# Optimization experiments

Hardware: AMD Instinct MI355X
Metric: run time of the kernel (lower is better)

The kernel has to match this reference:

```python
import jax, jax.numpy as jnp
import numpy as np

UNITS = 768
OUT_STEPS = 64
INPUT_DIM = 96


def setup_inputs() -> dict:
    key = jax.random.key(0)
    ks = jax.random.split(key, 7)
    B, T = 2048, 24
    s_ih = 1.0 / np.sqrt(UNITS)
    inputs = jax.random.normal(ks[0], (B, T, INPUT_DIM), dtype=jnp.float32)
    # PyTorch LSTMCell params: weight_ih [4U, I], weight_hh [4U, U], biases [4U]
    W_ih = jax.random.uniform(ks[1], (4 * UNITS, INPUT_DIM), minval=-s_ih, maxval=s_ih, dtype=jnp.float32)
    W_hh = jax.random.uniform(ks[2], (4 * UNITS, UNITS), minval=-s_ih, maxval=s_ih, dtype=jnp.float32)
    b_ih = jax.random.uniform(ks[3], (4 * UNITS,), minval=-s_ih, maxval=s_ih, dtype=jnp.float32)
    b_hh = jax.random.uniform(ks[4], (4 * UNITS,), minval=-s_ih, maxval=s_ih, dtype=jnp.float32)
    # Dense: Linear(units, input_dim)
    s_d = 1.0 / np.sqrt(UNITS)
    W_d = jax.random.uniform(ks[5], (INPUT_DIM, UNITS), minval=-s_d, maxval=s_d, dtype=jnp.float32)
    b_d = jax.random.uniform(ks[6], (INPUT_DIM,), minval=-s_d, maxval=s_d, dtype=jnp.float32)
    return {"inputs": inputs, "W_ih": W_ih, "W_hh": W_hh, "b_ih": b_ih, "b_hh": b_hh, "W_d": W_d, "b_d": b_d}


def _lstm_cell(x, h, c, W_ih, W_hh, b_ih, b_hh):
    # gates: [B, 4U], PyTorch gate order i, f, g, o
    gates = x @ W_ih.T + b_ih + h @ W_hh.T + b_hh
    i, f, g, o = jnp.split(gates, 4, axis=-1)
    i = jax.nn.sigmoid(i)
    f = jax.nn.sigmoid(f)
    g = jnp.tanh(g)
    o = jax.nn.sigmoid(o)
    c_new = f * c + i * g
    h_new = o * jnp.tanh(c_new)
    return h_new, c_new


def reference(inputs, W_ih, W_hh, b_ih, b_hh, W_d, b_d):
    B = inputs.shape[0]
    h0 = jnp.zeros((B, UNITS), dtype=inputs.dtype)
    c0 = jnp.zeros((B, UNITS), dtype=inputs.dtype)
    # warmup: feed last timestep
    x0 = inputs[:, -1, :]
    h, c = _lstm_cell(x0, h0, c0, W_ih, W_hh, b_ih, b_hh)
    pred0 = h @ W_d.T + b_d

    def step(carry, _):
        pred, h, c = carry
        h2, c2 = _lstm_cell(pred, h, c, W_ih, W_hh, b_ih, b_hh)
        pred2 = h2 @ W_d.T + b_d
        return (pred2, h2, c2), pred2

    _, preds_rest = jax.lax.scan(step, (pred0, h, c), None, length=OUT_STEPS - 1)
    # preds_rest: [out_steps-1, B, I] -> stack with pred0 along time axis 1
    preds = jnp.concatenate([pred0[None], preds_rest], axis=0)  # [out_steps, B, I]
    return jnp.transpose(preds, (1, 0, 2))  # [B, out_steps, I]
```

## Files before the change

### kernel.cpp

```cpp
#include <hip/hip_runtime.h>
#include <hip/hip_bf16.h>
#include <stdint.h>

typedef __hip_bfloat16 bf16_t;
typedef __attribute__((ext_vector_type(4))) float f32x4;
typedef __attribute__((ext_vector_type(8))) short s16x8;

#define UNITS 768
#define NCOLS 3072
#define NPRED 96
#define MROWS 2048

__device__ __forceinline__ float sigf(float x) {
    return __builtin_amdgcn_rcpf(1.f + __expf(-x));
}
__device__ __forceinline__ float tanh_fast(float x) {
    return 1.f - 2.f * __builtin_amdgcn_rcpf(1.f + __expf(2.f * x));
}


__global__ void prep_b0(const float* __restrict__ W_ih, bf16_t* __restrict__ B0T) {
    int idx = blockIdx.x * 256 + threadIdx.x;
    if (idx >= NCOLS * 96) return;
    int c = idx / 96, k = idx % 96;
    int u = ((c >> 6) << 4) + (c & 15);
    int g = (c >> 4) & 3;
    B0T[idx] = (bf16_t)W_ih[(g * UNITS + u) * 96 + k];
}

__global__ void prep_x0(const float* __restrict__ inputs, bf16_t* __restrict__ x0) {
    int idx = blockIdx.x * 256 + threadIdx.x;
    int j = idx & 7;
    int l = (idx >> 3) & 63;
    int fg = idx >> 9;
    int kf = fg % 3;
    int mf = fg / 3;
    int m = mf * 16 + (l & 15);
    int k = kf * 32 + (l >> 4) * 8 + j;
    x0[idx] = (bf16_t)inputs[(m * 24 + 23) * 96 + k];
}

__global__ void prep_bias(const float* __restrict__ b_ih, const float* __restrict__ b_hh,
                          const float* __restrict__ W_ih, const float* __restrict__ b_d,
                          float* __restrict__ b0_r, float* __restrict__ beff_r) {
    int c = blockIdx.x * 256 + threadIdx.x;
    if (c >= NCOLS) return;
    int u = ((c >> 6) << 4) + (c & 15);
    int g = (c >> 4) & 3;
    int r = g * UNITS + u;
    float v = b_ih[r] + b_hh[r];
    float acc = 0.f;
    for (int j = 0; j < 96; ++j) acc += W_ih[r * 96 + j] * b_d[j];
    b0_r[c] = v;
    beff_r[c] = v + acc;
}

__global__ void prep_beff2(const float* __restrict__ W_hh, const float* __restrict__ W_ih,
                           const float* __restrict__ W_d, bf16_t* __restrict__ BeffT) {
    __shared__ float sWih[64][96];
    __shared__ float sWd[96][64];
    const int c0 = blockIdx.x * 64, k0 = blockIdx.y * 64;
    const int tid = threadIdx.x;
    for (int i = tid; i < 64 * 96; i += 256) {
        int cc = i / 96, j = i % 96;
        int c = c0 + cc;
        int u = ((c >> 6) << 4) + (c & 15);
        int g = (c >> 4) & 3;
        sWih[cc][j] = W_ih[(g * UNITS + u) * 96 + j];
    }
    for (int i = tid; i < 96 * 64; i += 256) {
        int j = i / 64, kk = i % 64;
        sWd[j][kk] = W_d[j * UNITS + k0 + kk];
    }
    __syncthreads();
    const int kk = tid & 63;
    const int cc0 = (tid >> 6) * 16;
    for (int cc = cc0; cc < cc0 + 16; ++cc) {
        float acc = 0.f;
#pragma unroll 12
        for (int j = 0; j < 96; ++j) acc += sWih[cc][j] * sWd[j][kk];
        int c = c0 + cc;
        int u = ((c >> 6) << 4) + (c & 15);
        int g = (c >> 4) & 3;
        int r = g * UNITS + u;
        BeffT[(size_t)c * UNITS + k0 + kk] = (bf16_t)(W_hh[(size_t)r * UNITS + k0 + kk] + acc);
    }
}

__global__ void prep_wdt(const float* __restrict__ W_d, bf16_t* __restrict__ BeffT) {
    int idx = blockIdx.x * 256 + threadIdx.x;
    int c = idx / UNITS, k = idx % UNITS;
    float v = (c < NPRED) ? W_d[c * UNITS + k] : 0.f;
    BeffT[(size_t)(NCOLS + c) * UNITS + k] = (bf16_t)v;
}

__global__ void prep_swz(const bf16_t* __restrict__ src, bf16_t* __restrict__ dst,
                         int Knk, int K, int total) {
    int idx = blockIdx.x * 256 + threadIdx.x;
    if (idx >= total) return;
    int j = idx & 7;
    int l = (idx >> 3) & 63;
    int fg = idx >> 9;
    int f = fg & 3;
    int rest = fg >> 2;
    int kf = rest % Knk;
    int nw = rest / Knk;
    int c = (nw >> 1) * 128 + (nw & 1) * 64 + f * 16 + (l & 15);
    int k = kf * 32 + (l >> 4) * 8 + j;
    dst[idx] = src[(size_t)c * K + k];
}

__global__ void zero_ctr(int* __restrict__ c) {
    c[threadIdx.x] = 0;
}

__global__ __launch_bounds__(512, 2)
void lstm_persist(const bf16_t* __restrict__ x0s,
                  const bf16_t* __restrict__ B0s,
                  const bf16_t* __restrict__ Bs,
                  const float* __restrict__ b0r,
                  const float* __restrict__ beffr,
                  const float* __restrict__ b_d,
                  bf16_t* __restrict__ h0,
                  bf16_t* __restrict__ h1,
                  float* __restrict__ out,
                  int* __restrict__ ctr)
{
    __shared__ __align__(16) bf16_t smem[24 * 4 * 512];

    const int tid = threadIdx.x;
    const int wr   = tid >> 6;
    const int lane = tid & 63;
    const int l15 = lane & 15, l4 = lane >> 4;

    const int bid  = blockIdx.x;
    const int xcd  = bid & 7;
    const int ii   = bid >> 3;
    const int mt   = xcd >> 1;
    const int nt64 = (xcd & 1) * 25 + ii;
    const bool is_pred = (nt64 >= 48);
    const int nt  = nt64 >> 1;
    const int wcb = nt64 & 1;

    {
        const f32x4* src = (const f32x4*)(Bs + (size_t)nt64 * 49152);
        f32x4* dst = (f32x4*)smem;
        for (int i = tid; i < 6144; i += 512) dst[i] = src[i];
    }

    int aoffh[4], aoff0[4];
#pragma unroll
    for (int i = 0; i < 4; ++i) {
        int mf = mt * 32 + wr * 4 + i;
        aoffh[i] = (mf * 24) * 512 + lane * 8;
        aoff0[i] = (mf * 3) * 512 + lane * 8;
    }
    int boff0[4];
#pragma unroll
    for (int f = 0; f < 4; ++f)
        boff0[f] = ((nt64 * 12 + f) * 64 + lane) * 8;

    float bi0[4], biS[4];
    if (!is_pred) {
#pragma unroll
        for (int f = 0; f < 4; ++f) {
            int idx = nt * 128 + wcb * 64 + f * 16 + l15;
            bi0[f] = b0r[idx];
            biS[f] = beffr[idx];
        }
    } else {
#pragma unroll
        for (int f = 0; f < 4; ++f) {
            int j = wcb * 64 + f * 16 + l15;
            biS[f] = (j < NPRED) ? b_d[j] : 0.f;
            bi0[f] = 0.f;
        }
    }

    const int kq = wcb * 2 + (l15 >> 3);
    const int jj = l15 & 7;

    f32x4 creg[4];
#pragma unroll
    for (int i = 0; i < 4; ++i) creg[i] = f32x4{0.f, 0.f, 0.f, 0.f};

    int* cbase = ctr + mt * 64;

    f32x4 acc[4][4];

#define ZACC() do {                                                                  \
        _Pragma("unroll") for (int _i = 0; _i < 4; ++_i)                             \
        _Pragma("unroll") for (int _j = 0; _j < 4; ++_j)                             \
            acc[_i][_j] = f32x4{0.f, 0.f, 0.f, 0.f};                                 \
    } while (0)

#define LOADK_H(BUF, KT) do {                                                        \
        _Pragma("unroll")                                                            \
        for (int _i = 0; _i < 4; ++_i)                                               \
            afr[BUF][_i] = *(const s16x8*)(hA + aoffh[_i] + (size_t)(KT) * 512);     \
        _Pragma("unroll")                                                            \
        for (int _f = 0; _f < 4; ++_f)                                               \
            bfr[BUF][_f] = *(const s16x8*)(smem + ((KT) * 4 + _f) * 512 + lane * 8); \
    } while (0)

#define LOADK_0(BUF, KT) do {                                                        \
        _Pragma("unroll")                                                            \
        for (int _i = 0; _i < 4; ++_i)                                               \
            afr[BUF][_i] = *(const s16x8*)(x0s + aoff0[_i] + (size_t)(KT) * 512);    \
        _Pragma("unroll")                                                            \
        for (int _f = 0; _f < 4; ++_f)                                               \
            bfr[BUF][_f] = *(const s16x8*)(B0s + boff0[_f] + (size_t)(KT) * 2048);   \
    } while (0)

#define MF(BUF) do {                                                                 \
        _Pragma("unroll")                                                            \
        for (int _i = 0; _i < 4; ++_i)                                               \
            _Pragma("unroll")                                                        \
            for (int _j = 0; _j < 4; ++_j)                                           \
                acc[_i][_j] = __builtin_amdgcn_mfma_f32_16x16x32_bf16(               \
                    afr[BUF][_i], bfr[BUF][_j], acc[_i][_j], 0, 0, 0);               \
    } while (0)

#define RUN3(NK, LOADK) do {                                                         \
        s16x8 afr[3][4], bfr[3][4];                                                  \
        LOADK(0, 0); LOADK(1, 1);                                                    \
        const int _nk3 = (NK) / 3;                                                   \
        for (int _b3 = 0; _b3 < _nk3; ++_b3) {                                       \
            const int _kt = _b3 * 3;                                                 \
            if (_kt + 2 < (NK)) LOADK(2, _kt + 2);                                   \
            MF(0);                                                                   \
            if (_kt + 3 < (NK)) LOADK(0, _kt + 3);                                   \
            MF(1);                                                                   \
            if (_kt + 4 < (NK)) LOADK(1, _kt + 4);                                   \
            MF(2);                                                                   \
        }                                                                            \
    } while (0)

#define GATE_EPI(HW, BI) do {                                                        \
        _Pragma("unroll")                                                            \
        for (int _i = 0; _i < 4; ++_i) {                                             \
            const int _mf = mt * 32 + wr * 4 + _i;                                   \
            bf16_t* _hb = (HW) + (size_t)(_mf * 24 + nt) * 512;                      \
            _Pragma("unroll")                                                        \
            for (int _r = 0; _r < 4; ++_r) {                                         \
                float _gi = acc[_i][0][_r] + (BI)[0];                                \
                float _gf = acc[_i][1][_r] + (BI)[1];                                \
                float _gg = acc[_i][2][_r] + (BI)[2];                                \
                float _go = acc[_i][3][_r] + (BI)[3];                                \
                float _si = sigf(_gi);                                               \
                float _sf = sigf(_gf);                                               \
                float _tg = tanh_fast(_gg);                                          \
                float _so = sigf(_go);                                               \
                float _cn = _sf * creg[_i][_r] + _si * _tg;                          \
                creg[_i][_r] = _cn;                                                  \
                int _lp = (l4 * 4 + _r) | (kq << 4);                                 \
                _hb[_lp * 8 + jj] = (bf16_t)(_so * tanh_fast(_cn));                  \
            }                                                                        \
        }                                                                            \
    } while (0)

#define PRED_EPI(TCOL) do {                                                          \
        _Pragma("unroll")                                                            \
        for (int _f = 0; _f < 4; ++_f) {                                             \
            int _j = wcb * 64 + _f * 16 + l15;                                       \
            if (_j < NPRED) {                                                        \
                _Pragma("unroll")                                                    \
                for (int _i = 0; _i < 4; ++_i)                                       \
                    _Pragma("unroll")                                                \
                    for (int _r = 0; _r < 4; ++_r) {                                 \
                        int _row = mt * 512 + wr * 64 + _i * 16 + l4 * 4 + _r;       \
                        out[((size_t)_row * 64 + (TCOL)) * NPRED + _j] =             \
                            acc[_i][_f][_r] + biS[_f];                               \
                    }                                                                \
            }                                                                        \
        }                                                                            \
    } while (0)

    auto barrier_step = [&](int s) {
        __syncthreads();
        if (tid == 0) {
            if (is_pred) {
                __hip_atomic_fetch_add(cbase + s, 1, __ATOMIC_RELAXED,
                                       __HIP_MEMORY_SCOPE_AGENT);
            } else {
                __hip_atomic_fetch_add(cbase + s, 1, __ATOMIC_RELEASE,
                                       __HIP_MEMORY_SCOPE_AGENT);
            }
            int it = 0;
            while (__hip_atomic_load(cbase + s, __ATOMIC_RELAXED,
                                     __HIP_MEMORY_SCOPE_AGENT) < 50) {
                __builtin_amdgcn_s_sleep(8);
                if (++it > (1 << 24)) break;
            }
            (void)__hip_atomic_load(cbase + s, __ATOMIC_ACQUIRE,
                                    __HIP_MEMORY_SCOPE_AGENT);
        }
        __syncthreads();
    };

    if (!is_pred) {
        ZACC();
        RUN3(3, LOADK_0);
        GATE_EPI(h1, bi0);
    }
    barrier_step(0);

    for (int s = 1; s < 64; ++s) {
        const bf16_t* hA = (s & 1) ? h1 : h0;
        ZACC();
        RUN3(24, LOADK_H);
        if (!is_pred) {
            bf16_t* hW = ((s + 1) & 1) ? h1 : h0;
            GATE_EPI(hW, biS);
        } else {
            PRED_EPI(s - 1);
        }
        barrier_step(s);
    }

    if (is_pred) {
        const bf16_t* hA = h0;
        ZACC();
        RUN3(24, LOADK_H);
        PRED_EPI(63);
    }

#undef ZACC
#undef LOADK_H
#undef LOADK_0
#undef MF
#undef RUN3
#undef GATE_EPI
#undef PRED_EPI
}

extern "C" void kernel_launch(void* const* d_in, const int* in_sizes, int n_in,
                              void* d_out, int out_size, void* d_ws, size_t ws_size,
                              hipStream_t stream)
{
    const float* inputs = (const float*)d_in[0];
    const float* W_ih   = (const float*)d_in[1];
    const float* W_hh   = (const float*)d_in[2];
    const float* b_ih   = (const float*)d_in[3];
    const float* b_hh   = (const float*)d_in[4];
    const float* W_d    = (const float*)d_in[5];
    const float* b_d    = (const float*)d_in[6];
    float* out = (float*)d_out;

    char* ws = (char*)d_ws;
    size_t off = 0;
    auto alloc = [&](size_t bytes) -> char* {
        char* p = ws + off;
        off = (off + bytes + 255) & ~(size_t)255;
        return p;
    };
    bf16_t* B0T   = (bf16_t*)alloc((size_t)NCOLS * 96 * 2);
    bf16_t* B0s   = (bf16_t*)alloc((size_t)NCOLS * 96 * 2);
    bf16_t* BeffT = (bf16_t*)alloc((size_t)3200 * UNITS * 2);
    bf16_t* Bs    = (bf16_t*)alloc((size_t)3200 * UNITS * 2);
    bf16_t* x0s   = (bf16_t*)alloc((size_t)MROWS * 96 * 2);
    bf16_t* h0    = (bf16_t*)alloc((size_t)MROWS * UNITS * 2);
    bf16_t* h1    = (bf16_t*)alloc((size_t)MROWS * UNITS * 2);
    float*  b0r   = (float*)alloc(NCOLS * 4);
    float*  beffr = (float*)alloc(NCOLS * 4);
    int*    ctr   = (int*)alloc(256 * 4);

    prep_b0   <<<(NCOLS * 96 + 255) / 256, 256, 0, stream>>>(W_ih, B0T);
    prep_swz  <<<(NCOLS * 96 + 255) / 256, 256, 0, stream>>>(B0T, B0s, 3, 96, NCOLS * 96);
    prep_x0   <<<(MROWS * 96) / 256, 256, 0, stream>>>(inputs, x0s);
    prep_bias <<<(NCOLS + 255) / 256, 256, 0, stream>>>(b_ih, b_hh, W_ih, b_d, b0r, beffr);
    prep_beff2<<<dim3(48, 12), 256, 0, stream>>>(W_hh, W_ih, W_d, BeffT);
    prep_wdt  <<<(128 * UNITS) / 256, 256, 0, stream>>>(W_d, BeffT);
    prep_swz  <<<(3200 * UNITS + 255) / 256, 256, 0, stream>>>(BeffT, Bs, 24, UNITS, 3200 * UNITS);
    zero_ctr  <<<1, 256, 0, stream>>>(ctr);

    lstm_persist<<<200, 512, 0, stream>>>(x0s, B0s, Bs, b0r, beffr, b_d,
                                          h0, h1, out, ctr);

    (void)ws_size; (void)in_sizes; (void)n_in; (void)out_size;
}
```

Measured before the change: 1.299 ms.

## Retile persistent LSTM blocks to 128-column tiles with split LDS/global B operand

Each block now covers a full 128-column tile (both halves) for 256 rows across 8 row groups, instead of 64 columns by 512 rows over 4 groups. This changes the number of blocks that meet at each per-step barrier from 50 to 25. Three of the four B fragments per k-step stay in enlarged LDS, while the fourth is streamed from global memory. The k-loop pipeline also deepens from 3 to 4 buffers. The changes aim to cut barrier participants and give each block a larger share of the reused operand, at the cost of extra global traffic for the streamed fragment and more registers.

```diff
diff --git a/kernel.cpp b/kernel.cpp
--- a/kernel.cpp
+++ b/kernel.cpp
@@ -111,7 +111,8 @@
 }
 
 __global__ void zero_ctr(int* __restrict__ c) {
-    c[threadIdx.x] = 0;
+    int i = blockIdx.x * 256 + threadIdx.x;
+    if (i < 512) c[i] = 0;
 }
 
 __global__ __launch_bounds__(512, 2)
@@ -126,65 +127,75 @@
                   float* __restrict__ out,
                   int* __restrict__ ctr)
 {
-    __shared__ __align__(16) bf16_t smem[24 * 4 * 512];
+    __shared__ __align__(16) bf16_t smem[24 * 6 * 512];
 
     const int tid = threadIdx.x;
-    const int wr   = tid >> 6;
+    const int wv   = tid >> 6;
     const int lane = tid & 63;
+    const int wr = wv >> 1, wc = wv & 1;
     const int l15 = lane & 15, l4 = lane >> 4;
 
     const int bid  = blockIdx.x;
-    const int xcd  = bid & 7;
-    const int ii   = bid >> 3;
-    const int mt   = xcd >> 1;
-    const int nt64 = (xcd & 1) * 25 + ii;
-    const bool is_pred = (nt64 >= 48);
-    const int nt  = nt64 >> 1;
-    const int wcb = nt64 & 1;
+    const int grp  = bid & 7;
+    const int tile = bid >> 3;
+    const bool is_pred = (tile == 24);
+
+    const bf16_t* Bg = Bs + (size_t)(2 * tile + wc) * 49152;
 
     {
-        const f32x4* src = (const f32x4*)(Bs + (size_t)nt64 * 49152);
+        const f32x4* s0 = (const f32x4*)(Bs + (size_t)(2 * tile) * 49152);
+        const f32x4* s1 = (const f32x4*)(Bs + (size_t)(2 * tile + 1) * 49152);
         f32x4* dst = (f32x4*)smem;
-        for (int i = tid; i < 6144; i += 512) dst[i] = src[i];
+        for (int i = tid; i < 9216; i += 512) {
+            int l  = i & 63;
+            int ff = (i >> 6) % 6;
+            int kf = i / 384;
+            int f  = (ff >= 3) ? ff - 3 : ff;
+            const f32x4* src = (ff >= 3) ? s1 : s0;
+            dst[i] = src[(kf * 4 + f) * 64 + l];
+        }
     }
 
     int aoffh[4], aoff0[4];
 #pragma unroll
     for (int i = 0; i < 4; ++i) {
-        int mf = mt * 32 + wr * 4 + i;
+        int mf = grp * 16 + wr * 4 + i;
         aoffh[i] = (mf * 24) * 512 + lane * 8;
         aoff0[i] = (mf * 3) * 512 + lane * 8;
     }
     int boff0[4];
 #pragma unroll
     for (int f = 0; f < 4; ++f)
-        boff0[f] = ((nt64 * 12 + f) * 64 + lane) * 8;
+        boff0[f] = (((2 * tile + wc) * 12 + f) * 64 + lane) * 8;
+
+    const int ldsb = wc * 1536 + lane * 8;
+    const int bgof = 1536 + lane * 8;
 
     float bi0[4], biS[4];
     if (!is_pred) {
 #pragma unroll
         for (int f = 0; f < 4; ++f) {
-            int idx = nt * 128 + wcb * 64 + f * 16 + l15;
+            int idx = tile * 128 + wc * 64 + f * 16 + l15;
             bi0[f] = b0r[idx];
             biS[f] = beffr[idx];
         }
     } else {
 #pragma unroll
         for (int f = 0; f < 4; ++f) {
-            int j = wcb * 64 + f * 16 + l15;
+            int j = wc * 64 + f * 16 + l15;
             biS[f] = (j < NPRED) ? b_d[j] : 0.f;
             bi0[f] = 0.f;
         }
     }
 
-    const int kq = wcb * 2 + (l15 >> 3);
+    const int kq = wc * 2 + (l15 >> 3);
     const int jj = l15 & 7;
 
     f32x4 creg[4];
 #pragma unroll
     for (int i = 0; i < 4; ++i) creg[i] = f32x4{0.f, 0.f, 0.f, 0.f};
 
-    int* cbase = ctr + mt * 64;
+    int* cbase = ctr + grp * 64;
 
     f32x4 acc[4][4];
 
@@ -199,8 +210,9 @@
         for (int _i = 0; _i < 4; ++_i)                                               \
             afr[BUF][_i] = *(const s16x8*)(hA + aoffh[_i] + (size_t)(KT) * 512);     \
         _Pragma("unroll")                                                            \
-        for (int _f = 0; _f < 4; ++_f)                                               \
-            bfr[BUF][_f] = *(const s16x8*)(smem + ((KT) * 4 + _f) * 512 + lane * 8); \
+        for (int _f = 0; _f < 3; ++_f)                                               \
+            bfr[BUF][_f] = *(const s16x8*)(smem + ldsb + (KT) * 3072 + _f * 512);    \
+        bfr[BUF][3] = *(const s16x8*)(Bg + bgof + (size_t)(KT) * 2048);              \
     } while (0)
 
 #define LOADK_0(BUF, KT) do {                                                        \
@@ -221,26 +233,28 @@
                     afr[BUF][_i], bfr[BUF][_j], acc[_i][_j], 0, 0, 0);               \
     } while (0)
 
-#define RUN3(NK, LOADK) do {                                                         \
-        s16x8 afr[3][4], bfr[3][4];                                                  \
-        LOADK(0, 0); LOADK(1, 1);                                                    \
-        const int _nk3 = (NK) / 3;                                                   \
-        for (int _b3 = 0; _b3 < _nk3; ++_b3) {                                       \
-            const int _kt = _b3 * 3;                                                 \
-            if (_kt + 2 < (NK)) LOADK(2, _kt + 2);                                   \
+#define RUN4(NK, LOADK) do {                                                         \
+        s16x8 afr[4][4], bfr[4][4];                                                  \
+        LOADK(0, 0);                                                                 \
+        if (1 < (NK)) LOADK(1, 1);                                                   \
+        if (2 < (NK)) LOADK(2, 2);                                                   \
+        for (int _kt = 0; _kt < (NK); _kt += 4) {                                    \
+            if (_kt + 3 < (NK)) LOADK(3, _kt + 3);                                   \
             MF(0);                                                                   \
-            if (_kt + 3 < (NK)) LOADK(0, _kt + 3);                                   \
-            MF(1);                                                                   \
-            if (_kt + 4 < (NK)) LOADK(1, _kt + 4);                                   \
-            MF(2);                                                                   \
+            if (_kt + 4 < (NK)) LOADK(0, _kt + 4);                                   \
+            if (_kt + 1 < (NK)) MF(1);                                               \
+            if (_kt + 5 < (NK)) LOADK(1, _kt + 5);                                   \
+            if (_kt + 2 < (NK)) MF(2);                                               \
+            if (_kt + 6 < (NK)) LOADK(2, _kt + 6);                                   \
+            if (_kt + 3 < (NK)) MF(3);                                               \
         }                                                                            \
     } while (0)
 
 #define GATE_EPI(HW, BI) do {                                                        \
         _Pragma("unroll")                                                            \
         for (int _i = 0; _i < 4; ++_i) {                                             \
-            const int _mf = mt * 32 + wr * 4 + _i;                                   \
-            bf16_t* _hb = (HW) + (size_t)(_mf * 24 + nt) * 512;                      \
+            const int _mf = grp * 16 + wr * 4 + _i;                                  \
+            bf16_t* _hb = (HW) + (size_t)(_mf * 24 + tile) * 512;                    \
             _Pragma("unroll")                                                        \
             for (int _r = 0; _r < 4; ++_r) {                                         \
                 float _gi = acc[_i][0][_r] + (BI)[0];                                \
@@ -262,13 +276,13 @@
 #define PRED_EPI(TCOL) do {                                                          \
         _Pragma("unroll")                                                            \
         for (int _f = 0; _f < 4; ++_f) {                                             \
-            int _j = wcb * 64 + _f * 16 + l15;                                       \
+            int _j = wc * 64 + _f * 16 + l15;                                        \
             if (_j < NPRED) {                                                        \
                 _Pragma("unroll")                                                    \
                 for (int _i = 0; _i < 4; ++_i)                                       \
                     _Pragma("unroll")                                                \
                     for (int _r = 0; _r < 4; ++_r) {                                 \
-                        int _row = mt * 512 + wr * 64 + _i * 16 + l4 * 4 + _r;       \
+                        int _row = grp * 256 + wr * 64 + _i * 16 + l4 * 4 + _r;      \
                         out[((size_t)_row * 64 + (TCOL)) * NPRED + _j] =             \
                             acc[_i][_f][_r] + biS[_f];                               \
                     }                                                                \
@@ -288,9 +302,9 @@
             }
             int it = 0;
             while (__hip_atomic_load(cbase + s, __ATOMIC_RELAXED,
-                                     __HIP_MEMORY_SCOPE_AGENT) < 50) {
-                __builtin_amdgcn_s_sleep(8);
-                if (++it > (1 << 24)) break;
+                                     __HIP_MEMORY_SCOPE_AGENT) < 25) {
+                __builtin_amdgcn_s_sleep(4);
+                if (++it > (1 << 23)) break;
             }
             (void)__hip_atomic_load(cbase + s, __ATOMIC_ACQUIRE,
                                     __HIP_MEMORY_SCOPE_AGENT);
@@ -300,7 +314,7 @@
 
     if (!is_pred) {
         ZACC();
-        RUN3(3, LOADK_0);
+        RUN4(3, LOADK_0);
         GATE_EPI(h1, bi0);
     }
     barrier_step(0);
@@ -308,7 +322,7 @@
     for (int s = 1; s < 64; ++s) {
         const bf16_t* hA = (s & 1) ? h1 : h0;
         ZACC();
-        RUN3(24, LOADK_H);
+        RUN4(24, LOADK_H);
         if (!is_pred) {
             bf16_t* hW = ((s + 1) & 1) ? h1 : h0;
             GATE_EPI(hW, biS);
@@ -321,7 +335,7 @@
     if (is_pred) {
         const bf16_t* hA = h0;
         ZACC();
-        RUN3(24, LOADK_H);
+        RUN4(24, LOADK_H);
         PRED_EPI(63);
     }
 
@@ -329,7 +343,7 @@
 #undef LOADK_H
 #undef LOADK_0
 #undef MF
-#undef RUN3
+#undef RUN4
 #undef GATE_EPI
 #undef PRED_EPI
 }
@@ -363,7 +377,7 @@
     bf16_t* h1    = (bf16_t*)alloc((size_t)MROWS * UNITS * 2);
     float*  b0r   = (float*)alloc(NCOLS * 4);
     float*  beffr = (float*)alloc(NCOLS * 4);
-    int*    ctr   = (int*)alloc(256 * 4);
+    int*    ctr   = (int*)alloc(512 * 4);
 
     prep_b0   <<<(NCOLS * 96 + 255) / 256, 256, 0, stream>>>(W_ih, B0T);
     prep_swz  <<<(NCOLS * 96 + 255) / 256, 256, 0, stream>>>(B0T, B0s, 3, 96, NCOLS * 96);
@@ -372,7 +386,7 @@
     prep_beff2<<<dim3(48, 12), 256, 0, stream>>>(W_hh, W_ih, W_d, BeffT);
     prep_wdt  <<<(128 * UNITS) / 256, 256, 0, stream>>>(W_d, BeffT);
     prep_swz  <<<(3200 * UNITS + 255) / 256, 256, 0, stream>>>(BeffT, Bs, 24, UNITS, 3200 * UNITS);
-    zero_ctr  <<<1, 256, 0, stream>>>(ctr);
+    zero_ctr  <<<2, 256, 0, stream>>>(ctr);
 
     lstm_persist<<<200, 512, 0, stream>>>(x0s, B0s, Bs, b0r, beffr, b_d,
                                           h0, h1, out, ctr);
```

Result: slower. 1.578 ms (+21.5%).
